# Performance work log

Hardware: AMD Instinct MI355X
Metric: run time of the kernel (lower is better)

The kernel has to match this reference:

```python
import jax, jax.numpy as jnp
import numpy as np

ALPHA = 0.5
N_NODES = 100000
N_EDGES = 1600000
D_IN = 128
D_OUT = 128


def setup_inputs() -> dict:
    key = jax.random.key(0)
    k1, k2, k3, k4, k5, k6 = jax.random.split(key, 6)
    x = jax.random.normal(k1, (N_NODES, D_IN), dtype=jnp.float32)
    edge_index = jax.random.randint(k2, (2, N_EDGES), 0, N_NODES, dtype=jnp.int64)
    # torch Linear default init: U(-1/sqrt(fan_in), 1/sqrt(fan_in)); scale similar here
    s = 1.0 / np.sqrt(D_IN)
    W_src = jax.random.uniform(k3, (D_OUT, D_IN), jnp.float32, -s, s)
    b_src = jax.random.uniform(k4, (D_OUT,), jnp.float32, -s, s)
    W_dst = jax.random.uniform(k5, (D_OUT, D_IN), jnp.float32, -s, s)
    b_dst = jax.random.uniform(k6, (D_OUT,), jnp.float32, -s, s)
    return {"x": x, "edge_index": edge_index, "W_src": W_src, "b_src": b_src,
            "W_dst": W_dst, "b_dst": b_dst}


def _inv_sqrt(deg):
    # deg^{-1/2} with inf -> 0 (isolated nodes)
    return jnp.where(deg > 0, jax.lax.rsqrt(jnp.maximum(deg, 1e-30)), 0.0)


def reference(x, edge_index, W_src, b_src, W_dst, b_dst):
    n = x.shape[0]
    row, col = edge_index[0], edge_index[1]
    ones = jnp.ones(row.shape[0], dtype=x.dtype)
    # degrees of directed adjacency A[row, col] = 1
    deg_out = jax.ops.segment_sum(ones, row, num_segments=n)  # row sums
    deg_in = jax.ops.segment_sum(ones, col, num_segments=n)   # col sums
    # D_out^{-1/2} A D_in^{-1/2} edge weights; transpose norm yields the SAME weights
    w = _inv_sqrt(deg_out)[row] * _inv_sqrt(deg_in)[col]      # [E]
    # adj_norm @ x : aggregate sources (col) into destinations (row)
    agg_fwd = jax.ops.segment_sum(w[:, None] * x[col], row, num_segments=n)  # [N, D_IN]
    # adj_t_norm @ x : aggregate destinations (row) into sources (col)
    agg_bwd = jax.ops.segment_sum(w[:, None] * x[row], col, num_segments=n)  # [N, D_IN]
    out = ALPHA * (agg_fwd @ W_src.T + b_src) + (1.0 - ALPHA) * (agg_bwd @ W_dst.T + b_dst)
    return out
```

## Files before the change

### kernel.cpp

```cpp
#include <hip/hip_runtime.h>
#include <stdint.h>

#define D 128
#define CE 2048
#define CAP 5120

typedef __attribute__((ext_vector_type(8))) __bf16 bf16x8;
typedef __attribute__((ext_vector_type(4))) float floatx4;

union FragU { uint4 u; bf16x8 b; };

__device__ __forceinline__ float bf16_lo(uint32_t u) { return __uint_as_float(u << 16); }
__device__ __forceinline__ float bf16_hi(uint32_t u) { return __uint_as_float(u & 0xffff0000u); }
__device__ __forceinline__ uint16_t f32_to_bf16(float f) {
    uint32_t u = __float_as_uint(f);
    uint32_t r = u + 0x7fffu + ((u >> 16) & 1u);
    return (uint16_t)(r >> 16);
}
__device__ __forceinline__ uint32_t pack2(float a, float b) {
    return (uint32_t)f32_to_bf16(a) | ((uint32_t)f32_to_bf16(b) << 16);
}

__global__ __launch_bounds__(256) void k_init(uint32_t* __restrict__ gcursor, int nb2)
{
    for (int j = threadIdx.x + blockIdx.x * 256; j < nb2; j += gridDim.x * 256)
        gcursor[j] = (uint32_t)j * CAP;
}

__global__ __launch_bounds__(256) void k_part(
    const int* __restrict__ ei, int E, int nbuk,
    uint32_t* __restrict__ gcursor, uint32_t* __restrict__ gpairs)
{
    __shared__ uint32_t cnt[1024];
    __shared__ uint32_t loff[1024];
    __shared__ uint32_t gbase[1024];
    __shared__ uint32_t spair[2 * CE];
    __shared__ uint16_t sbid[2 * CE];
    __shared__ uint32_t ssum[256];
    int nb2 = 2 * nbuk;
    for (int j = threadIdx.x; j < nb2; j += 256) cnt[j] = 0;
    __syncthreads();
    int base = blockIdx.x * CE;
    int lim = min(CE, E - base);
    for (int i = threadIdx.x; i < lim; i += 256) {
        int r = ei[base + i];
        int c = ei[E + base + i];
        atomicAdd(&cnt[r >> 8], 1u);
        atomicAdd(&cnt[nbuk + (c >> 8)], 1u);
    }
    __syncthreads();
    uint32_t v0 = 0, v1 = 0, v2 = 0, v3 = 0;
    int b0 = threadIdx.x * 4;
    if (b0 < nb2)     v0 = cnt[b0];
    if (b0 + 1 < nb2) v1 = cnt[b0 + 1];
    if (b0 + 2 < nb2) v2 = cnt[b0 + 2];
    if (b0 + 3 < nb2) v3 = cnt[b0 + 3];
    uint32_t tsum = v0 + v1 + v2 + v3;
    ssum[threadIdx.x] = tsum;
    __syncthreads();
    for (int off = 1; off < 256; off <<= 1) {
        uint32_t t = (threadIdx.x >= (unsigned)off) ? ssum[threadIdx.x - off] : 0u;
        __syncthreads();
        ssum[threadIdx.x] += t;
        __syncthreads();
    }
    uint32_t run = ssum[threadIdx.x] - tsum;
    if (b0 < nb2)     loff[b0]     = run;
    if (b0 + 1 < nb2) loff[b0 + 1] = run + v0;
    if (b0 + 2 < nb2) loff[b0 + 2] = run + v0 + v1;
    if (b0 + 3 < nb2) loff[b0 + 3] = run + v0 + v1 + v2;
    __syncthreads();
    for (int j = threadIdx.x; j < nb2; j += 256) {
        uint32_t c2 = cnt[j];
        gbase[j] = c2 ? atomicAdd(&gcursor[j], c2) : 0u;
        cnt[j] = loff[j];
    }
    __syncthreads();
    for (int i = threadIdx.x; i < lim; i += 256) {
        int r = ei[base + i];
        int c = ei[E + base + i];
        int bf = r >> 8;
        uint32_t sf = atomicAdd(&cnt[bf], 1u);
        spair[sf] = ((uint32_t)c << 8) | (uint32_t)(r & 255);
        sbid[sf] = (uint16_t)bf;
        int bb = nbuk + (c >> 8);
        uint32_t sb = atomicAdd(&cnt[bb], 1u);
        spair[sb] = ((uint32_t)r << 8) | (uint32_t)(c & 255);
        sbid[sb] = (uint16_t)bb;
    }
    __syncthreads();
    int total = 2 * lim;
    for (int s2 = threadIdx.x; s2 < total; s2 += 256) {
        int b = sbid[s2];
        gpairs[gbase[b] + ((uint32_t)s2 - loff[b])] = spair[s2];
    }
}

__global__ __launch_bounds__(256) void k_build(
    const uint32_t* __restrict__ gpairs, const uint32_t* __restrict__ gcursor,
    int nbuk, int N,
    int* __restrict__ edata, uint32_t* __restrict__ ptrg, uint32_t* __restrict__ degg,
    float* __restrict__ inv_o, float* __restrict__ inv_i)
{
    __shared__ uint32_t hist[256], cur[256], ssum[256];
    int b = blockIdx.x;
    int dir = (b >= nbuk) ? 1 : 0;
    int node0 = (b - dir * nbuk) << 8;
    uint32_t base = (uint32_t)b * CAP;
    uint32_t cnt_b = gcursor[b] - base;
    hist[threadIdx.x] = 0;
    __syncthreads();
    for (uint32_t i = threadIdx.x; i < cnt_b; i += 256)
        atomicAdd(&hist[gpairs[base + i] & 255u], 1u);
    __syncthreads();
    uint32_t h = hist[threadIdx.x];
    ssum[threadIdx.x] = h;
    __syncthreads();
    for (int off = 1; off < 256; off <<= 1) {
        uint32_t t = (threadIdx.x >= (unsigned)off) ? ssum[threadIdx.x - off] : 0u;
        __syncthreads();
        ssum[threadIdx.x] += t;
        __syncthreads();
    }
    uint32_t excl = ssum[threadIdx.x] - h;
    cur[threadIdx.x] = excl;
    int n = node0 + threadIdx.x;
    if (n < N) {
        ptrg[dir * N + n] = base + excl;
        degg[dir * N + n] = h;
        float iv = h ? rsqrtf((float)h) : 0.0f;
        if (dir == 0) inv_o[n] = iv; else inv_i[n] = iv;
    }
    __syncthreads();
    for (uint32_t i = threadIdx.x; i < cnt_b; i += 256) {
        uint32_t e = gpairs[base + i];
        uint32_t pos = atomicAdd(&cur[e & 255u], 1u);
        edata[base + pos] = (int)(e >> 8);
    }
}

__global__ __launch_bounds__(256) void k_mm(
    const float* __restrict__ x,
    const float* __restrict__ Wsrc, const float* __restrict__ Wdst,
    const float* __restrict__ inv_o, const float* __restrict__ inv_i,
    uint32_t* __restrict__ u2, uint32_t* __restrict__ v2, int N)
{
    __shared__ uint4 sWf[2048];
    const int lane = threadIdx.x & 63;
    const int m16 = lane & 15;
    const int quad = lane >> 4;
    const int mat = blockIdx.x & 1;
    uint32_t* outb = mat ? v2 : u2;
    const float* inv = mat ? inv_o : inv_i;
    const float* Wm = mat ? Wdst : Wsrc;

    {
        uint32_t* sW32 = (uint32_t*)sWf;
        for (int idx = threadIdx.x; idx < 8192; idx += 256) {
            int slot = idx >> 2, j2 = idx & 3;
            int ct = slot >> 8, ks = (slot >> 6) & 3, qd = (slot >> 4) & 3, mm = slot & 15;
            const float2 w = *(const float2*)(Wm + (ct * 16 + mm) * 128 + ks * 32 + qd * 8 + 2 * j2);
            sW32[idx] = pack2(0.5f * w.x, 0.5f * w.y);
        }
    }
    __syncthreads();

    const int ntiles = (N + 15) >> 4;
    const int wslot = (blockIdx.x >> 1) * 4 + (threadIdx.x >> 6);
    const int nslot = (gridDim.x >> 1) * 4;

    for (int t = wslot; t < ntiles; t += nslot) {
        int node = t * 16 + m16;
        int rowA = node < N ? node : N - 1;
        const float4* xr = (const float4*)(x + (long)rowA * 128);
        bf16x8 Xf[4];
        #pragma unroll
        for (int ks = 0; ks < 4; ++ks) {
            float4 p0 = xr[ks * 8 + quad * 2];
            float4 p1 = xr[ks * 8 + quad * 2 + 1];
            FragU f;
            f.u.x = pack2(p0.x, p0.y);
            f.u.y = pack2(p0.z, p0.w);
            f.u.z = pack2(p1.x, p1.y);
            f.u.w = pack2(p1.z, p1.w);
            Xf[ks] = f.b;
        }
        float iv = inv[rowA];
        bool ok = (node < N);
        #pragma unroll
        for (int ct = 0; ct < 8; ++ct) {
            floatx4 acc = {};
            #pragma unroll
            for (int ks = 0; ks < 4; ++ks) {
                FragU wf; wf.u = sWf[ct * 256 + ks * 64 + lane];
                acc = __builtin_amdgcn_mfma_f32_16x16x32_bf16(wf.b, Xf[ks], acc, 0, 0, 0);
            }
            if (ok) {
                uint2 val;
                val.x = pack2(acc[0] * iv, acc[1] * iv);
                val.y = pack2(acc[2] * iv, acc[3] * iv);
                *(uint2*)(outb + (long)node * 64 + ct * 8 + quad * 2) = val;
            }
        }
    }
}

__global__ __launch_bounds__(256) void k_gather(
    const uint32_t* __restrict__ u2, const uint32_t* __restrict__ v2,
    const int* __restrict__ edata,
    const uint32_t* __restrict__ ptrg, const uint32_t* __restrict__ degg,
    const float* __restrict__ inv_out, const float* __restrict__ inv_in,
    const float* __restrict__ bsrc, const float* __restrict__ bdst,
    float* __restrict__ out, int N, int nStart, int nEnd)
{
    const int lane = threadIdx.x & 63;
    const int h = lane >> 5;
    const int j = lane & 31;
    int node = nStart + blockIdx.x * 4 + (threadIdx.x >> 6);
    if (node >= nEnd) return;

    uint32_t s0 = ptrg[node],     d0 = degg[node];
    uint32_t s1 = ptrg[N + node], d1 = degg[N + node];
    float io = inv_out[node], ii = inv_in[node];
    const float4 bs = *(const float4*)(bsrc + 4 * j);
    const float4 bd = *(const float4*)(bdst + 4 * j);

    float f0 = 0, f1 = 0, f2 = 0, f3 = 0;
    {
        uint32_t k = 0;
        for (; k + 8 <= d0; k += 8) {
            int i0 = edata[s0 + k     + h];
            int i1 = edata[s0 + k + 2 + h];
            int i2 = edata[s0 + k + 4 + h];
            int i3 = edata[s0 + k + 6 + h];
            uint2 p0 = *(const uint2*)(u2 + (long)i0 * 64 + 2 * j);
            uint2 p1 = *(const uint2*)(u2 + (long)i1 * 64 + 2 * j);
            uint2 p2 = *(const uint2*)(u2 + (long)i2 * 64 + 2 * j);
            uint2 p3 = *(const uint2*)(u2 + (long)i3 * 64 + 2 * j);
            f0 += bf16_lo(p0.x) + bf16_lo(p1.x) + bf16_lo(p2.x) + bf16_lo(p3.x);
            f1 += bf16_hi(p0.x) + bf16_hi(p1.x) + bf16_hi(p2.x) + bf16_hi(p3.x);
            f2 += bf16_lo(p0.y) + bf16_lo(p1.y) + bf16_lo(p2.y) + bf16_lo(p3.y);
            f3 += bf16_hi(p0.y) + bf16_hi(p1.y) + bf16_hi(p2.y) + bf16_hi(p3.y);
        }
        for (; k + 2 <= d0; k += 2) {
            int i0 = edata[s0 + k + h];
            uint2 p = *(const uint2*)(u2 + (long)i0 * 64 + 2 * j);
            f0 += bf16_lo(p.x); f1 += bf16_hi(p.x);
            f2 += bf16_lo(p.y); f3 += bf16_hi(p.y);
        }
        if (k < d0 && h == 0) {
            int i0 = edata[s0 + k];
            uint2 p = *(const uint2*)(u2 + (long)i0 * 64 + 2 * j);
            f0 += bf16_lo(p.x); f1 += bf16_hi(p.x);
            f2 += bf16_lo(p.y); f3 += bf16_hi(p.y);
        }
    }

    float g0 = 0, g1 = 0, g2 = 0, g3 = 0;
    {
        uint32_t k = 0;
        for (; k + 8 <= d1; k += 8) {
            int i0 = edata[s1 + k     + h];
            int i1 = edata[s1 + k + 2 + h];
            int i2 = edata[s1 + k + 4 + h];
            int i3 = edata[s1 + k + 6 + h];
            uint2 p0 = *(const uint2*)(v2 + (long)i0 * 64 + 2 * j);
            uint2 p1 = *(const uint2*)(v2 + (long)i1 * 64 + 2 * j);
            uint2 p2 = *(const uint2*)(v2 + (long)i2 * 64 + 2 * j);
            uint2 p3 = *(const uint2*)(v2 + (long)i3 * 64 + 2 * j);
            g0 += bf16_lo(p0.x) + bf16_lo(p1.x) + bf16_lo(p2.x) + bf16_lo(p3.x);
            g1 += bf16_hi(p0.x) + bf16_hi(p1.x) + bf16_hi(p2.x) + bf16_hi(p3.x);
            g2 += bf16_lo(p0.y) + bf16_lo(p1.y) + bf16_lo(p2.y) + bf16_lo(p3.y);
            g3 += bf16_hi(p0.y) + bf16_hi(p1.y) + bf16_hi(p2.y) + bf16_hi(p3.y);
        }
        for (; k + 2 <= d1; k += 2) {
            int i0 = edata[s1 + k + h];
            uint2 p = *(const uint2*)(v2 + (long)i0 * 64 + 2 * j);
            g0 += bf16_lo(p.x); g1 += bf16_hi(p.x);
            g2 += bf16_lo(p.y); g3 += bf16_hi(p.y);
        }
        if (k < d1 && h == 0) {
            int i0 = edata[s1 + k];
            uint2 p = *(const uint2*)(v2 + (long)i0 * 64 + 2 * j);
            g0 += bf16_lo(p.x); g1 += bf16_hi(p.x);
            g2 += bf16_lo(p.y); g3 += bf16_hi(p.y);
        }
    }

    f0 += __shfl_xor(f0, 32); f1 += __shfl_xor(f1, 32);
    f2 += __shfl_xor(f2, 32); f3 += __shfl_xor(f3, 32);
    g0 += __shfl_xor(g0, 32); g1 += __shfl_xor(g1, 32);
    g2 += __shfl_xor(g2, 32); g3 += __shfl_xor(g3, 32);

    if (h == 0) {
        float4 o;
        o.x = io * f0 + ii * g0 + 0.5f * (bs.x + bd.x);
        o.y = io * f1 + ii * g1 + 0.5f * (bs.y + bd.y);
        o.z = io * f2 + ii * g2 + 0.5f * (bs.z + bd.z);
        o.w = io * f3 + ii * g3 + 0.5f * (bs.w + bd.w);
        *(float4*)(out + (long)node * 128 + 4 * j) = o;
    }
}

extern "C" void kernel_launch(void* const* d_in, const int* in_sizes, int n_in,
                              void* d_out, int out_size, void* d_ws, size_t ws_size,
                              hipStream_t stream) {
    const int N = in_sizes[0] / D;
    const int E = in_sizes[1] / 2;
    const int nbuk = (N + 255) >> 8;
    const int nb2 = 2 * nbuk;

    const float* x    = (const float*)d_in[0];
    const int*   ei   = (const int*)d_in[1];
    const float* Wsrc = (const float*)d_in[2];
    const float* bsrc = (const float*)d_in[3];
    const float* Wdst = (const float*)d_in[4];
    const float* bdst = (const float*)d_in[5];

    char* ws = (char*)d_ws;
    size_t off = 0;
    uint32_t* gcur   = (uint32_t*)(ws + off); off += 1024 * 4;
    float*    inv_o  = (float*)(ws + off);    off += (size_t)N * 4;
    float*    inv_i  = (float*)(ws + off);    off += (size_t)N * 4;
    uint32_t* ptrg   = (uint32_t*)(ws + off); off += (size_t)2 * N * 4;
    uint32_t* degg   = (uint32_t*)(ws + off); off += (size_t)2 * N * 4;
    uint32_t* gpairs = (uint32_t*)(ws + off); off += (size_t)nb2 * CAP * 4;
    int*      edata  = (int*)(ws + off);      off += (size_t)nb2 * CAP * 4;
    uint32_t* u2     = (uint32_t*)(ws + off); off += (size_t)N * 64 * 4;
    uint32_t* v2     = (uint32_t*)(ws + off); off += (size_t)N * 64 * 4;

    k_init<<<4, 256, 0, stream>>>(gcur, nb2);

    k_part<<<(E + CE - 1) / CE, 256, 0, stream>>>(ei, E, nbuk, gcur, gpairs);

    k_build<<<nb2, 256, 0, stream>>>(gpairs, gcur, nbuk, N,
                                     edata, ptrg, degg, inv_o, inv_i);

    k_mm<<<2048, 256, 0, stream>>>(x, Wsrc, Wdst, inv_o, inv_i, u2, v2, N);

    int half = (N + 1) / 2;
    k_gather<<<(half + 3) / 4, 256, 0, stream>>>(u2, v2, edata, ptrg, degg,
                                                 inv_o, inv_i, bsrc, bdst,
                                                 (float*)d_out, N, 0, half);
    k_gather<<<(N - half + 3) / 4, 256, 0, stream>>>(u2, v2, edata, ptrg, degg,
                                                     inv_o, inv_i, bsrc, bdst,
                                                     (float*)d_out, N, half, N);
}
```

Before: 334.2 us.

## Compute both projections per X tile in k_mm and grid-stride gather kernel

The matmul kernel now loads both weight matrices into shared memory and computes the src and dst projections from a single load of each X tile. Before, each block handled only one matrix, so X was read twice. The gather kernel becomes persistent with a fixed grid of 2048 blocks that loop over nodes, which cuts block launch overhead. The cost is doubled LDS use per block (64KB), which lowers occupancy in k_mm, and a fixed gather grid that may balance load across nodes less evenly.

```diff
diff --git a/kernel.cpp b/kernel.cpp
--- a/kernel.cpp
+++ b/kernel.cpp
@@ -145,20 +145,19 @@
     const float* __restrict__ inv_o, const float* __restrict__ inv_i,
     uint32_t* __restrict__ u2, uint32_t* __restrict__ v2, int N)
 {
-    __shared__ uint4 sWf[2048];
+    __shared__ uint4 sWf[4096];
     const int lane = threadIdx.x & 63;
     const int m16 = lane & 15;
     const int quad = lane >> 4;
-    const int mat = blockIdx.x & 1;
-    uint32_t* outb = mat ? v2 : u2;
-    const float* inv = mat ? inv_o : inv_i;
-    const float* Wm = mat ? Wdst : Wsrc;
 
     {
         uint32_t* sW32 = (uint32_t*)sWf;
-        for (int idx = threadIdx.x; idx < 8192; idx += 256) {
-            int slot = idx >> 2, j2 = idx & 3;
+        for (int idx = threadIdx.x; idx < 16384; idx += 256) {
+            int mat = idx >> 13;
+            int rid = idx & 8191;
+            int slot = rid >> 2, j2 = rid & 3;
             int ct = slot >> 8, ks = (slot >> 6) & 3, qd = (slot >> 4) & 3, mm = slot & 15;
+            const float* Wm = mat ? Wdst : Wsrc;
             const float2 w = *(const float2*)(Wm + (ct * 16 + mm) * 128 + ks * 32 + qd * 8 + 2 * j2);
             sW32[idx] = pack2(0.5f * w.x, 0.5f * w.y);
         }
@@ -166,8 +165,8 @@
     __syncthreads();
 
     const int ntiles = (N + 15) >> 4;
-    const int wslot = (blockIdx.x >> 1) * 4 + (threadIdx.x >> 6);
-    const int nslot = (gridDim.x >> 1) * 4;
+    const int wslot = blockIdx.x * 4 + (threadIdx.x >> 6);
+    const int nslot = gridDim.x * 4;
 
     for (int t = wslot; t < ntiles; t += nslot) {
         int node = t * 16 + m16;
@@ -185,21 +184,27 @@
             f.u.w = pack2(p1.z, p1.w);
             Xf[ks] = f.b;
         }
-        float iv = inv[rowA];
+        float ivu = inv_i[rowA];
+        float ivv = inv_o[rowA];
         bool ok = (node < N);
         #pragma unroll
         for (int ct = 0; ct < 8; ++ct) {
-            floatx4 acc = {};
+            floatx4 a0 = {}, a1 = {};
             #pragma unroll
             for (int ks = 0; ks < 4; ++ks) {
-                FragU wf; wf.u = sWf[ct * 256 + ks * 64 + lane];
-                acc = __builtin_amdgcn_mfma_f32_16x16x32_bf16(wf.b, Xf[ks], acc, 0, 0, 0);
+                FragU w0; w0.u = sWf[ct * 256 + ks * 64 + lane];
+                a0 = __builtin_amdgcn_mfma_f32_16x16x32_bf16(w0.b, Xf[ks], a0, 0, 0, 0);
+                FragU w1; w1.u = sWf[2048 + ct * 256 + ks * 64 + lane];
+                a1 = __builtin_amdgcn_mfma_f32_16x16x32_bf16(w1.b, Xf[ks], a1, 0, 0, 0);
             }
             if (ok) {
-                uint2 val;
-                val.x = pack2(acc[0] * iv, acc[1] * iv);
-                val.y = pack2(acc[2] * iv, acc[3] * iv);
-                *(uint2*)(outb + (long)node * 64 + ct * 8 + quad * 2) = val;
+                uint2 val0, val1;
+                val0.x = pack2(a0[0] * ivu, a0[1] * ivu);
+                val0.y = pack2(a0[2] * ivu, a0[3] * ivu);
+                val1.x = pack2(a1[0] * ivv, a1[1] * ivv);
+                val1.y = pack2(a1[2] * ivv, a1[3] * ivv);
+                *(uint2*)(u2 + (long)node * 64 + ct * 8 + quad * 2) = val0;
+                *(uint2*)(v2 + (long)node * 64 + ct * 8 + quad * 2) = val1;
             }
         }
     }
@@ -216,89 +221,91 @@
     const int lane = threadIdx.x & 63;
     const int h = lane >> 5;
     const int j = lane & 31;
-    int node = nStart + blockIdx.x * 4 + (threadIdx.x >> 6);
-    if (node >= nEnd) return;
-
-    uint32_t s0 = ptrg[node],     d0 = degg[node];
-    uint32_t s1 = ptrg[N + node], d1 = degg[N + node];
-    float io = inv_out[node], ii = inv_in[node];
     const float4 bs = *(const float4*)(bsrc + 4 * j);
     const float4 bd = *(const float4*)(bdst + 4 * j);
-
-    float f0 = 0, f1 = 0, f2 = 0, f3 = 0;
-    {
-        uint32_t k = 0;
-        for (; k + 8 <= d0; k += 8) {
-            int i0 = edata[s0 + k     + h];
-            int i1 = edata[s0 + k + 2 + h];
-            int i2 = edata[s0 + k + 4 + h];
-            int i3 = edata[s0 + k + 6 + h];
-            uint2 p0 = *(const uint2*)(u2 + (long)i0 * 64 + 2 * j);
-            uint2 p1 = *(const uint2*)(u2 + (long)i1 * 64 + 2 * j);
-            uint2 p2 = *(const uint2*)(u2 + (long)i2 * 64 + 2 * j);
-            uint2 p3 = *(const uint2*)(u2 + (long)i3 * 64 + 2 * j);
-            f0 += bf16_lo(p0.x) + bf16_lo(p1.x) + bf16_lo(p2.x) + bf16_lo(p3.x);
-            f1 += bf16_hi(p0.x) + bf16_hi(p1.x) + bf16_hi(p2.x) + bf16_hi(p3.x);
-            f2 += bf16_lo(p0.y) + bf16_lo(p1.y) + bf16_lo(p2.y) + bf16_lo(p3.y);
-            f3 += bf16_hi(p0.y) + bf16_hi(p1.y) + bf16_hi(p2.y) + bf16_hi(p3.y);
-        }
-        for (; k + 2 <= d0; k += 2) {
-            int i0 = edata[s0 + k + h];
-            uint2 p = *(const uint2*)(u2 + (long)i0 * 64 + 2 * j);
-            f0 += bf16_lo(p.x); f1 += bf16_hi(p.x);
-            f2 += bf16_lo(p.y); f3 += bf16_hi(p.y);
-        }
-        if (k < d0 && h == 0) {
-            int i0 = edata[s0 + k];
-            uint2 p = *(const uint2*)(u2 + (long)i0 * 64 + 2 * j);
-            f0 += bf16_lo(p.x); f1 += bf16_hi(p.x);
-            f2 += bf16_lo(p.y); f3 += bf16_hi(p.y);
-        }
-    }
-
-    float g0 = 0, g1 = 0, g2 = 0, g3 = 0;
-    {
-        uint32_t k = 0;
-        for (; k + 8 <= d1; k += 8) {
-            int i0 = edata[s1 + k     + h];
-            int i1 = edata[s1 + k + 2 + h];
-            int i2 = edata[s1 + k + 4 + h];
-            int i3 = edata[s1 + k + 6 + h];
-            uint2 p0 = *(const uint2*)(v2 + (long)i0 * 64 + 2 * j);
-            uint2 p1 = *(const uint2*)(v2 + (long)i1 * 64 + 2 * j);
-            uint2 p2 = *(const uint2*)(v2 + (long)i2 * 64 + 2 * j);
-            uint2 p3 = *(const uint2*)(v2 + (long)i3 * 64 + 2 * j);
-            g0 += bf16_lo(p0.x) + bf16_lo(p1.x) + bf16_lo(p2.x) + bf16_lo(p3.x);
-            g1 += bf16_hi(p0.x) + bf16_hi(p1.x) + bf16_hi(p2.x) + bf16_hi(p3.x);
-            g2 += bf16_lo(p0.y) + bf16_lo(p1.y) + bf16_lo(p2.y) + bf16_lo(p3.y);
-            g3 += bf16_hi(p0.y) + bf16_hi(p1.y) + bf16_hi(p2.y) + bf16_hi(p3.y);
-        }
-        for (; k + 2 <= d1; k += 2) {
-            int i0 = edata[s1 + k + h];
-            uint2 p = *(const uint2*)(v2 + (long)i0 * 64 + 2 * j);
-            g0 += bf16_lo(p.x); g1 += bf16_hi(p.x);
-            g2 += bf16_lo(p.y); g3 += bf16_hi(p.y);
-        }
-        if (k < d1 && h == 0) {
-            int i0 = edata[s1 + k];
-            uint2 p = *(const uint2*)(v2 + (long)i0 * 64 + 2 * j);
-            g0 += bf16_lo(p.x); g1 += bf16_hi(p.x);
-            g2 += bf16_lo(p.y); g3 += bf16_hi(p.y);
-        }
-    }
-
-    f0 += __shfl_xor(f0, 32); f1 += __shfl_xor(f1, 32);
-    f2 += __shfl_xor(f2, 32); f3 += __shfl_xor(f3, 32);
-    g0 += __shfl_xor(g0, 32); g1 += __shfl_xor(g1, 32);
-    g2 += __shfl_xor(g2, 32); g3 += __shfl_xor(g3, 32);
-
-    if (h == 0) {
-        float4 o;
-        o.x = io * f0 + ii * g0 + 0.5f * (bs.x + bd.x);
-        o.y = io * f1 + ii * g1 + 0.5f * (bs.y + bd.y);
-        o.z = io * f2 + ii * g2 + 0.5f * (bs.z + bd.z);
-        o.w = io * f3 + ii * g3 + 0.5f * (bs.w + bd.w);
-        *(float4*)(out + (long)node * 128 + 4 * j) = o;
+    const int wid = blockIdx.x * 4 + (threadIdx.x >> 6);
+    const int nw = gridDim.x * 4;
+
+    for (int node = nStart + wid; node < nEnd; node += nw) {
+        uint32_t s0 = ptrg[node],     d0 = degg[node];
+        uint32_t s1 = ptrg[N + node], d1 = degg[N + node];
+        float io = inv_out[node], ii = inv_in[node];
+
+        float f0 = 0, f1 = 0, f2 = 0, f3 = 0;
+        {
+            uint32_t k = 0;
+            for (; k + 8 <= d0; k += 8) {
+                int i0 = edata[s0 + k     + h];
+                int i1 = edata[s0 + k + 2 + h];
+                int i2 = edata[s0 + k + 4 + h];
+                int i3 = edata[s0 + k + 6 + h];
+                uint2 p0 = *(const uint2*)(u2 + (long)i0 * 64 + 2 * j);
+                uint2 p1 = *(const uint2*)(u2 + (long)i1 * 64 + 2 * j);
+                uint2 p2 = *(const uint2*)(u2 + (long)i2 * 64 + 2 * j);
+                uint2 p3 = *(const uint2*)(u2 + (long)i3 * 64 + 2 * j);
+                f0 += bf16_lo(p0.x) + bf16_lo(p1.x) + bf16_lo(p2.x) + bf16_lo(p3.x);
+                f1 += bf16_hi(p0.x) + bf16_hi(p1.x) + bf16_hi(p2.x) + bf16_hi(p3.x);
+                f2 += bf16_lo(p0.y) + bf16_lo(p1.y) + bf16_lo(p2.y) + bf16_lo(p3.y);
+                f3 += bf16_hi(p0.y) + bf16_hi(p1.y) + bf16_hi(p2.y) + bf16_hi(p3.y);
+            }
+            for (; k + 2 <= d0; k += 2) {
+                int i0 = edata[s0 + k + h];
+                uint2 p = *(const uint2*)(u2 + (long)i0 * 64 + 2 * j);
+                f0 += bf16_lo(p.x); f1 += bf16_hi(p.x);
+                f2 += bf16_lo(p.y); f3 += bf16_hi(p.y);
+            }
+            if (k < d0 && h == 0) {
+                int i0 = edata[s0 + k];
+                uint2 p = *(const uint2*)(u2 + (long)i0 * 64 + 2 * j);
+                f0 += bf16_lo(p.x); f1 += bf16_hi(p.x);
+                f2 += bf16_lo(p.y); f3 += bf16_hi(p.y);
+            }
+        }
+
+        float g0 = 0, g1 = 0, g2 = 0, g3 = 0;
+        {
+            uint32_t k = 0;
+            for (; k + 8 <= d1; k += 8) {
+                int i0 = edata[s1 + k     + h];
+                int i1 = edata[s1 + k + 2 + h];
+                int i2 = edata[s1 + k + 4 + h];
+                int i3 = edata[s1 + k + 6 + h];
+                uint2 p0 = *(const uint2*)(v2 + (long)i0 * 64 + 2 * j);
+                uint2 p1 = *(const uint2*)(v2 + (long)i1 * 64 + 2 * j);
+                uint2 p2 = *(const uint2*)(v2 + (long)i2 * 64 + 2 * j);
+                uint2 p3 = *(const uint2*)(v2 + (long)i3 * 64 + 2 * j);
+                g0 += bf16_lo(p0.x) + bf16_lo(p1.x) + bf16_lo(p2.x) + bf16_lo(p3.x);
+                g1 += bf16_hi(p0.x) + bf16_hi(p1.x) + bf16_hi(p2.x) + bf16_hi(p3.x);
+                g2 += bf16_lo(p0.y) + bf16_lo(p1.y) + bf16_lo(p2.y) + bf16_lo(p3.y);
+                g3 += bf16_hi(p0.y) + bf16_hi(p1.y) + bf16_hi(p2.y) + bf16_hi(p3.y);
+            }
+            for (; k + 2 <= d1; k += 2) {
+                int i0 = edata[s1 + k + h];
+                uint2 p = *(const uint2*)(v2 + (long)i0 * 64 + 2 * j);
+                g0 += bf16_lo(p.x); g1 += bf16_hi(p.x);
+                g2 += bf16_lo(p.y); g3 += bf16_hi(p.y);
+            }
+            if (k < d1 && h == 0) {
+                int i0 = edata[s1 + k];
+                uint2 p = *(const uint2*)(v2 + (long)i0 * 64 + 2 * j);
+                g0 += bf16_lo(p.x); g1 += bf16_hi(p.x);
+                g2 += bf16_lo(p.y); g3 += bf16_hi(p.y);
+            }
+        }
+
+        f0 += __shfl_xor(f0, 32); f1 += __shfl_xor(f1, 32);
+        f2 += __shfl_xor(f2, 32); f3 += __shfl_xor(f3, 32);
+        g0 += __shfl_xor(g0, 32); g1 += __shfl_xor(g1, 32);
+        g2 += __shfl_xor(g2, 32); g3 += __shfl_xor(g3, 32);
+
+        if (h == 0) {
+            float4 o;
+            o.x = io * f0 + ii * g0 + 0.5f * (bs.x + bd.x);
+            o.y = io * f1 + ii * g1 + 0.5f * (bs.y + bd.y);
+            o.z = io * f2 + ii * g2 + 0.5f * (bs.z + bd.z);
+            o.w = io * f3 + ii * g3 + 0.5f * (bs.w + bd.w);
+            *(float4*)(out + (long)node * 128 + 4 * j) = o;
+        }
     }
 }
 
@@ -336,13 +343,13 @@
     k_build<<<nb2, 256, 0, stream>>>(gpairs, gcur, nbuk, N,
                                      edata, ptrg, degg, inv_o, inv_i);
 
-    k_mm<<<2048, 256, 0, stream>>>(x, Wsrc, Wdst, inv_o, inv_i, u2, v2, N);
+    k_mm<<<1024, 256, 0, stream>>>(x, Wsrc, Wdst, inv_o, inv_i, u2, v2, N);
 
     int half = (N + 1) / 2;
-    k_gather<<<(half + 3) / 4, 256, 0, stream>>>(u2, v2, edata, ptrg, degg,
-                                                 inv_o, inv_i, bsrc, bdst,
-                                                 (float*)d_out, N, 0, half);
-    k_gather<<<(N - half + 3) / 4, 256, 0, stream>>>(u2, v2, edata, ptrg, degg,
-                                                     inv_o, inv_i, bsrc, bdst,
-                                                     (float*)d_out, N, half, N);
-}
+    k_gather<<<2048, 256, 0, stream>>>(u2, v2, edata, ptrg, degg,
+                                       inv_o, inv_i, bsrc, bdst,
+                                       (float*)d_out, N, 0, half);
+    k_gather<<<2048, 256, 0, stream>>>(u2, v2, edata, ptrg, degg,
+                                       inv_o, inv_i, bsrc, bdst,
+                                       (float*)d_out, N, half, N);
+}
```

New measurement: 349.9 us. 4.7% more time.
